# Kernel tuning notes

Hardware: AMD Instinct MI355X
Metric: run time of the kernel (lower is better)

Reference implementation:

```python
import jax, jax.numpy as jnp
import numpy as np

LAMBD = 1.0  # margin, matches init kwarg lambd
N, C, D = 16384, 4096, 128


def setup_inputs() -> dict:
    key = jax.random.key(0)
    k1, k2, k3 = jax.random.split(key, 3)
    embeddings = jax.random.normal(k1, (N, D), dtype=jnp.float32)
    targets = jax.random.randint(k2, (N,), 0, C, dtype=jnp.int64)
    centers = jax.random.normal(k3, (C, D), dtype=jnp.float32)
    return {"embeddings": embeddings, "targets": targets, "centers": centers}


def reference(embeddings, targets, centers):
    # Squared euclidean distances from every sample to every center, [n, C],
    # via ||e||^2 + ||c||^2 - 2 e.c (avoids the [n, C, d] broadcast tensor).
    e2 = jnp.sum(embeddings * embeddings, axis=-1, keepdims=True)          # [n, 1]
    c2 = jnp.sum(centers * centers, axis=-1)                               # [C]
    dist = e2 + c2[None, :] - 2.0 * jnp.matmul(embeddings, centers.T)      # [n, C]

    tgt = targets.astype(jnp.int32)
    ap = jnp.take_along_axis(dist, tgt[:, None], axis=1)                   # [n, 1]

    # loss_val[i, c] = lambd + d(e_i, center_{y_i}) - d(e_i, center_c)
    loss_val = LAMBD + ap - dist                                           # [n, C]

    # Triplet (i, y_i, c) is mined iff loss_val > 0 and c != y_i.
    not_label = jnp.arange(dist.shape[1], dtype=jnp.int32)[None, :] != tgt[:, None]
    mask = (loss_val > 0.0) & not_label

    # For mined triplets relu(ap - an + lambd) == loss_val (already > 0).
    total = jnp.sum(jnp.where(mask, loss_val, 0.0))
    cnt = jnp.sum(mask).astype(loss_val.dtype)
    # If no triplet violates the margin, the original returns 0.
    return jnp.where(cnt > 0.0, total / jnp.maximum(cnt, 1.0), 0.0)
```

## Files before the change

### kernel.cpp

```cpp
#include <hip/hip_runtime.h>

#define N_SAMP 16384
#define N_CENT 4096
#define DIM    128
#define LAMBD  1.0f
#define NSLOT  256

typedef _Float16 half8  __attribute__((ext_vector_type(8)));
typedef float    floatx4 __attribute__((ext_vector_type(4)));

struct Slot { float sum; unsigned int cnt; unsigned int pad[30]; };

__device__ __forceinline__ void gload_lds16(const void* g, void* l) {
  __builtin_amdgcn_global_load_lds(
      (__attribute__((address_space(1))) void*)(g),
      (__attribute__((address_space(3))) void*)(l), 16, 0, 0);
}

__global__ __launch_bounds__(256) void prep_kernel(
    const float* __restrict__ E, const float* __restrict__ Cc,
    const int* __restrict__ tgt,
    _Float16* __restrict__ Eh, _Float16* __restrict__ Ch,
    float* __restrict__ c2, float* __restrict__ rowk,
    Slot* __restrict__ slots) {
  const int tid = threadIdx.x;
  const int STAT_BLOCKS = (N_SAMP + N_CENT) / 4;
  if ((int)blockIdx.x < STAT_BLOCKS) {
    if (blockIdx.x == 0) { slots[tid].sum = 0.f; slots[tid].cnt = 0u; }
    const int wv   = blockIdx.x * 4 + (tid >> 6);
    const int lane = tid & 63;
    if (wv < N_SAMP) {
      const int yi = tgt[wv];
      float2 e = *(const float2*)(E  + (size_t)wv * DIM + lane * 2);
      float2 c = *(const float2*)(Cc + (size_t)yi * DIM + lane * 2);
      float s = c.x * (c.x - 2.f * e.x) + c.y * (c.y - 2.f * e.y);
      #pragma unroll
      for (int off = 32; off > 0; off >>= 1) s += __shfl_down(s, off);
      if (lane == 0) rowk[wv] = LAMBD + s;
    } else {
      const int cI = wv - N_SAMP;
      float2 c = *(const float2*)(Cc + (size_t)cI * DIM + lane * 2);
      float s = c.x * c.x + c.y * c.y;
      #pragma unroll
      for (int off = 32; off > 0; off >>= 1) s += __shfl_down(s, off);
      if (lane == 0) c2[cI] = s;
    }
  } else {
    const int t = ((int)blockIdx.x - STAT_BLOCKS) * 256 + tid;
    const int NE8 = N_SAMP * DIM / 8;
    const float4* src;
    half8* dst;
    int idx;
    if (t < NE8) { src = (const float4*)E;  dst = (half8*)Eh; idx = t; }
    else         { src = (const float4*)Cc; dst = (half8*)Ch; idx = t - NE8; }
    float4 a = src[(size_t)idx * 2], b = src[(size_t)idx * 2 + 1];
    half8 h;
    h[0]=(_Float16)a.x; h[1]=(_Float16)a.y; h[2]=(_Float16)a.z; h[3]=(_Float16)a.w;
    h[4]=(_Float16)b.x; h[5]=(_Float16)b.y; h[6]=(_Float16)b.z; h[7]=(_Float16)b.w;
    dst[idx] = h;
  }
}

__global__ __launch_bounds__(256, 2) void center_gemm_kernel(
    const _Float16* __restrict__ Eh, const _Float16* __restrict__ Ch,
    const float* __restrict__ c2, const float* __restrict__ rowk,
    const int* __restrict__ tgt,
    Slot* __restrict__ slots) {
  __shared__ _Float16 As[128 * DIM];
  __shared__ _Float16 Bs[128 * DIM];
  __shared__ float rowkS[128];
  __shared__ float c2S[128];
  __shared__ int   yS[128];
  __shared__ float swsum[4];
  __shared__ int   swcnt[4];

  const int tid  = threadIdx.x;
  const int w    = tid >> 6;
  const int lane = tid & 63;

  const int bid = blockIdx.x;
  const int xcd = bid & 7;
  const int j   = bid >> 3;
  const int bm  = xcd * 16 + (j & 15);
  const int bn  = j >> 4;

  {
    const char* gA = (const char*)(Eh + (size_t)bm * 128 * DIM);
    const char* gB = (const char*)(Ch + (size_t)bn * 128 * DIM);
    char* lA = (char*)As;
    char* lB = (char*)Bs;
    const int p  = lane & 15;
    const int r4 = lane >> 4;
    #pragma unroll
    for (int it = 0; it < 8; ++it) {
      const int off = (w * 8 + it) * 1024;
      const int row = (w * 8 + it) * 4 + r4;
      const int gof = row * 256 + (p ^ (row & 15)) * 16;
      gload_lds16(gA + gof, lA + off);
      gload_lds16(gB + gof, lB + off);
    }
  }
  if (tid < 128) {
    rowkS[tid] = rowk[bm * 128 + tid];
    yS[tid]    = tgt[bm * 128 + tid];
    c2S[tid]   = c2[bn * 128 + tid];
  }
  __syncthreads();

  const int wm = w >> 1, wn = w & 1;
  const int q = lane >> 4, r = lane & 15;
  const int row0 = wm * 64, col0 = wn * 64;

  floatx4 acc[4][4];
  #pragma unroll
  for (int a = 0; a < 4; ++a)
    #pragma unroll
    for (int b = 0; b < 4; ++b)
      acc[a][b] = (floatx4){0.f, 0.f, 0.f, 0.f};

  #pragma unroll
  for (int ks = 0; ks < 4; ++ks) {
    const int cidx = ks * 4 + q;
    half8 af[4], bf[4];
    #pragma unroll
    for (int mt = 0; mt < 4; ++mt)
      af[mt] = *(const half8*)&As[(row0 + mt * 16 + r) * DIM + ((cidx ^ r) * 8)];
    #pragma unroll
    for (int nt = 0; nt < 4; ++nt)
      bf[nt] = *(const half8*)&Bs[(col0 + nt * 16 + r) * DIM + ((cidx ^ r) * 8)];
    #pragma unroll
    for (int mt = 0; mt < 4; ++mt)
      #pragma unroll
      for (int nt = 0; nt < 4; ++nt)
        acc[mt][nt] = __builtin_amdgcn_mfma_f32_16x16x32_f16(af[mt], bf[nt], acc[mt][nt], 0, 0, 0);
  }

  float lsum = 0.f;
  int   lcnt = 0;
  #pragma unroll
  for (int mt = 0; mt < 4; ++mt) {
    float rk[4]; int yv[4];
    #pragma unroll
    for (int rg = 0; rg < 4; ++rg) {
      const int row = row0 + mt * 16 + q * 4 + rg;
      rk[rg] = rowkS[row];
      yv[rg] = yS[row];
    }
    #pragma unroll
    for (int nt = 0; nt < 4; ++nt) {
      const int col  = col0 + nt * 16 + r;
      const float c2v = c2S[col];
      const int gcol = bn * 128 + col;
      #pragma unroll
      for (int rg = 0; rg < 4; ++rg) {
        const float v = rk[rg] + 2.f * acc[mt][nt][rg] - c2v;
        const bool mined = (v > 0.f) & (gcol != yv[rg]);
        lsum += mined ? v : 0.f;
        lcnt += mined ? 1 : 0;
      }
    }
  }

  #pragma unroll
  for (int off = 32; off > 0; off >>= 1) {
    lsum += __shfl_down(lsum, off);
    lcnt += __shfl_down(lcnt, off);
  }
  if (lane == 0) { swsum[w] = lsum; swcnt[w] = lcnt; }
  __syncthreads();
  if (tid == 0) {
    const float s = swsum[0] + swsum[1] + swsum[2] + swsum[3];
    const int   c = swcnt[0] + swcnt[1] + swcnt[2] + swcnt[3];
    Slot* sl = &slots[bid & (NSLOT - 1)];
    atomicAdd(&sl->sum, s);
    atomicAdd(&sl->cnt, (unsigned int)c);
  }
}

__global__ __launch_bounds__(256) void finalize_kernel(
    const Slot* __restrict__ slots, float* __restrict__ out) {
  const int tid = threadIdx.x;
  float s = slots[tid].sum;
  unsigned int c = slots[tid].cnt;
  #pragma unroll
  for (int off = 32; off > 0; off >>= 1) {
    s += __shfl_down(s, off);
    c += __shfl_down(c, off);
  }
  __shared__ float ss[4];
  __shared__ unsigned int sc[4];
  if ((tid & 63) == 0) { ss[tid >> 6] = s; sc[tid >> 6] = c; }
  __syncthreads();
  if (tid == 0) {
    const float S = ss[0] + ss[1] + ss[2] + ss[3];
    const unsigned int C = sc[0] + sc[1] + sc[2] + sc[3];
    out[0] = (C > 0u) ? (S / (float)C) : 0.f;
  }
}

__global__ void zero_kernel(float* ws_sum, unsigned int* ws_cnt) {
  if (threadIdx.x == 0) { *ws_sum = 0.f; *ws_cnt = 0u; }
}

__global__ void finalize_simple(const float* __restrict__ ws_sum,
                                const unsigned int* __restrict__ ws_cnt,
                                float* __restrict__ out) {
  if (threadIdx.x == 0 && blockIdx.x == 0) {
    const unsigned int c = *ws_cnt;
    out[0] = (c > 0u) ? (*ws_sum / (float)c) : 0.f;
  }
}

__global__ __launch_bounds__(256) void fallback_kernel(
    const float* __restrict__ E, const float* __restrict__ Cc,
    const int* __restrict__ tgt,
    float* __restrict__ ws_sum, unsigned int* __restrict__ ws_cnt) {
  __shared__ float eS[DIM];
  __shared__ float apS;
  const int i = blockIdx.x;
  const int tid = threadIdx.x;
  if (tid < DIM) eS[tid] = E[(size_t)i * DIM + tid];
  __syncthreads();
  const int yi = tgt[i];
  float dloc[16];
  #pragma unroll
  for (int j = 0; j < 16; ++j) {
    const int c = tid + 256 * j;
    const float* cp = Cc + (size_t)c * DIM;
    float s = 0.f;
    for (int d = 0; d < DIM; d += 4) {
      float4 cv = *(const float4*)(cp + d);
      s += cv.x * (cv.x - 2.f * eS[d + 0]) + cv.y * (cv.y - 2.f * eS[d + 1])
         + cv.z * (cv.z - 2.f * eS[d + 2]) + cv.w * (cv.w - 2.f * eS[d + 3]);
    }
    dloc[j] = s;
    if (c == yi) apS = s;
  }
  __syncthreads();
  const float apv = apS;
  float lsum = 0.f; int lcnt = 0;
  #pragma unroll
  for (int j = 0; j < 16; ++j) {
    const int c = tid + 256 * j;
    const float v = LAMBD + apv - dloc[j];
    const bool mined = (v > 0.f) & (c != yi);
    lsum += mined ? v : 0.f;
    lcnt += mined ? 1 : 0;
  }
  #pragma unroll
  for (int off = 32; off > 0; off >>= 1) {
    lsum += __shfl_down(lsum, off);
    lcnt += __shfl_down(lcnt, off);
  }
  __shared__ float swsum[4];
  __shared__ int   swcnt[4];
  const int w = tid >> 6, lane = tid & 63;
  if (lane == 0) { swsum[w] = lsum; swcnt[w] = lcnt; }
  __syncthreads();
  if (tid == 0) {
    atomicAdd(ws_sum, swsum[0] + swsum[1] + swsum[2] + swsum[3]);
    atomicAdd(ws_cnt, (unsigned int)(swcnt[0] + swcnt[1] + swcnt[2] + swcnt[3]));
  }
}

extern "C" void kernel_launch(void* const* d_in, const int* in_sizes, int n_in,
                              void* d_out, int out_size, void* d_ws, size_t ws_size,
                              hipStream_t stream) {
  const float* E   = (const float*)d_in[0];
  const int*   tgt = (const int*)d_in[1];
  const float* Cc  = (const float*)d_in[2];
  float* out = (float*)d_out;

  const size_t EH_BYTES = (size_t)N_SAMP * DIM * 2;
  const size_t CH_BYTES = (size_t)N_CENT * DIM * 2;
  const size_t C2_BYTES = (size_t)N_CENT * 4;
  const size_t RK_BYTES = (size_t)N_SAMP * 4;
  const size_t SL_BYTES = (size_t)NSLOT * sizeof(Slot);
  const size_t NEEDED = EH_BYTES + CH_BYTES + C2_BYTES + RK_BYTES + SL_BYTES;

  char* ws = (char*)d_ws;
  if (ws_size >= NEEDED) {
    _Float16* Eh = (_Float16*)ws;
    _Float16* Ch = (_Float16*)(ws + EH_BYTES);
    float* c2    = (float*)(ws + EH_BYTES + CH_BYTES);
    float* rowk  = (float*)(ws + EH_BYTES + CH_BYTES + C2_BYTES);
    Slot* slots  = (Slot*)(ws + EH_BYTES + CH_BYTES + C2_BYTES + RK_BYTES);

    const int STAT_BLOCKS = (N_SAMP + N_CENT) / 4;
    const int CONV_BLOCKS = (N_SAMP * DIM / 8 + N_CENT * DIM / 8) / 256;
    prep_kernel<<<STAT_BLOCKS + CONV_BLOCKS, 256, 0, stream>>>(
        E, Cc, tgt, Eh, Ch, c2, rowk, slots);
    center_gemm_kernel<<<(N_CENT / 128) * (N_SAMP / 128), 256, 0, stream>>>(
        Eh, Ch, c2, rowk, tgt, slots);
    finalize_kernel<<<1, 256, 0, stream>>>(slots, out);
  } else {
    float* ws_sum = (float*)ws;
    unsigned int* ws_cnt = (unsigned int*)(ws_sum + 1);
    zero_kernel<<<1, 64, 0, stream>>>(ws_sum, ws_cnt);
    fallback_kernel<<<N_SAMP, 256, 0, stream>>>(E, Cc, tgt, ws_sum, ws_cnt);
    finalize_simple<<<1, 64, 0, stream>>>(ws_sum, ws_cnt, out);
  }
}
```

Measured before the change: 101.3 us.

## Make GEMM blocks persistent over eight row tiles with double-buffered A loads

```diff
diff --git a/kernel.cpp b/kernel.cpp
--- a/kernel.cpp
+++ b/kernel.cpp
@@ -61,104 +61,134 @@
   }
 }
 
-__global__ __launch_bounds__(256, 2) void center_gemm_kernel(
+__global__ __launch_bounds__(512, 2) void center_gemm_kernel(
     const _Float16* __restrict__ Eh, const _Float16* __restrict__ Ch,
     const float* __restrict__ c2, const float* __restrict__ rowk,
     const int* __restrict__ tgt,
     Slot* __restrict__ slots) {
-  __shared__ _Float16 As[128 * DIM];
-  __shared__ _Float16 Bs[128 * DIM];
-  __shared__ float rowkS[128];
-  __shared__ float c2S[128];
-  __shared__ int   yS[128];
-  __shared__ float swsum[4];
-  __shared__ int   swcnt[4];
+  __shared__ _Float16 As[2][128 * DIM];
+  __shared__ _Float16 Bs[256 * DIM];
+  __shared__ float c2S[256];
+  __shared__ float rowkS[2][128];
+  __shared__ int   yS[2][128];
+  __shared__ float swsum[8];
+  __shared__ int   swcnt[8];
 
   const int tid  = threadIdx.x;
   const int w    = tid >> 6;
   const int lane = tid & 63;
 
-  const int bid = blockIdx.x;
-  const int xcd = bid & 7;
-  const int j   = bid >> 3;
-  const int bm  = xcd * 16 + (j & 15);
-  const int bn  = j >> 4;
+  const int bid    = blockIdx.x;
+  const int xcd    = bid & 7;
+  const int j      = bid >> 3;
+  const int bm_grp = xcd * 2 + (j & 1);
+  const int bn_grp = j >> 1;
+  const int bn0    = bn_grp * 256;
+
+  const int p  = lane & 15;
+  const int r4 = lane >> 4;
 
   {
-    const char* gA = (const char*)(Eh + (size_t)bm * 128 * DIM);
-    const char* gB = (const char*)(Ch + (size_t)bn * 128 * DIM);
-    char* lA = (char*)As;
+    const char* gB = (const char*)(Ch + (size_t)bn0 * DIM);
     char* lB = (char*)Bs;
-    const int p  = lane & 15;
-    const int r4 = lane >> 4;
     #pragma unroll
     for (int it = 0; it < 8; ++it) {
-      const int off = (w * 8 + it) * 1024;
-      const int row = (w * 8 + it) * 4 + r4;
-      const int gof = row * 256 + (p ^ (row & 15)) * 16;
-      gload_lds16(gA + gof, lA + off);
-      gload_lds16(gB + gof, lB + off);
-    }
-  }
+      const int chunk = w * 8 + it;
+      const int row   = chunk * 4 + r4;
+      gload_lds16(gB + row * 256 + (p ^ (row & 15)) * 16, lB + chunk * 1024);
+    }
+    const char* gA = (const char*)(Eh + (size_t)bm_grp * 8 * 128 * DIM);
+    char* lA = (char*)As[0];
+    #pragma unroll
+    for (int it = 0; it < 4; ++it) {
+      const int chunk = w * 4 + it;
+      const int row   = chunk * 4 + r4;
+      gload_lds16(gA + row * 256 + (p ^ (row & 15)) * 16, lA + chunk * 1024);
+    }
+  }
+  if (tid < 256) c2S[tid] = c2[bn0 + tid];
   if (tid < 128) {
-    rowkS[tid] = rowk[bm * 128 + tid];
-    yS[tid]    = tgt[bm * 128 + tid];
-    c2S[tid]   = c2[bn * 128 + tid];
-  }
-  __syncthreads();
-
-  const int wm = w >> 1, wn = w & 1;
+    const int rg0 = bm_grp * 8 * 128 + tid;
+    rowkS[0][tid] = rowk[rg0];
+    yS[0][tid]    = tgt[rg0];
+  }
+  __syncthreads();
+
+  const int wm = w >> 2, wn = w & 3;
   const int q = lane >> 4, r = lane & 15;
   const int row0 = wm * 64, col0 = wn * 64;
 
-  floatx4 acc[4][4];
-  #pragma unroll
-  for (int a = 0; a < 4; ++a)
-    #pragma unroll
-    for (int b = 0; b < 4; ++b)
-      acc[a][b] = (floatx4){0.f, 0.f, 0.f, 0.f};
-
-  #pragma unroll
-  for (int ks = 0; ks < 4; ++ks) {
-    const int cidx = ks * 4 + q;
-    half8 af[4], bf[4];
-    #pragma unroll
-    for (int mt = 0; mt < 4; ++mt)
-      af[mt] = *(const half8*)&As[(row0 + mt * 16 + r) * DIM + ((cidx ^ r) * 8)];
-    #pragma unroll
-    for (int nt = 0; nt < 4; ++nt)
-      bf[nt] = *(const half8*)&Bs[(col0 + nt * 16 + r) * DIM + ((cidx ^ r) * 8)];
-    #pragma unroll
-    for (int mt = 0; mt < 4; ++mt)
-      #pragma unroll
-      for (int nt = 0; nt < 4; ++nt)
-        acc[mt][nt] = __builtin_amdgcn_mfma_f32_16x16x32_f16(af[mt], bf[nt], acc[mt][nt], 0, 0, 0);
-  }
-
   float lsum = 0.f;
   int   lcnt = 0;
-  #pragma unroll
-  for (int mt = 0; mt < 4; ++mt) {
-    float rk[4]; int yv[4];
-    #pragma unroll
-    for (int rg = 0; rg < 4; ++rg) {
-      const int row = row0 + mt * 16 + q * 4 + rg;
-      rk[rg] = rowkS[row];
-      yv[rg] = yS[row];
-    }
-    #pragma unroll
-    for (int nt = 0; nt < 4; ++nt) {
-      const int col  = col0 + nt * 16 + r;
-      const float c2v = c2S[col];
-      const int gcol = bn * 128 + col;
+
+  for (int t = 0; t < 8; ++t) {
+    const int cur = t & 1;
+
+    if (t < 7) {
+      const char* gA = (const char*)(Eh + (size_t)(bm_grp * 8 + t + 1) * 128 * DIM);
+      char* lA = (char*)As[cur ^ 1];
+      #pragma unroll
+      for (int it = 0; it < 4; ++it) {
+        const int chunk = w * 4 + it;
+        const int row   = chunk * 4 + r4;
+        gload_lds16(gA + row * 256 + (p ^ (row & 15)) * 16, lA + chunk * 1024);
+      }
+      if (tid < 128) {
+        const int rg1 = (bm_grp * 8 + t + 1) * 128 + tid;
+        rowkS[cur ^ 1][tid] = rowk[rg1];
+        yS[cur ^ 1][tid]    = tgt[rg1];
+      }
+    }
+
+    floatx4 acc[4][4];
+    #pragma unroll
+    for (int a = 0; a < 4; ++a)
+      #pragma unroll
+      for (int b = 0; b < 4; ++b)
+        acc[a][b] = (floatx4){0.f, 0.f, 0.f, 0.f};
+
+    #pragma unroll
+    for (int ks = 0; ks < 4; ++ks) {
+      const int cidx = ks * 4 + q;
+      half8 af[4], bf[4];
+      #pragma unroll
+      for (int mt = 0; mt < 4; ++mt)
+        af[mt] = *(const half8*)&As[cur][(row0 + mt * 16 + r) * DIM + ((cidx ^ r) * 8)];
+      #pragma unroll
+      for (int nt = 0; nt < 4; ++nt)
+        bf[nt] = *(const half8*)&Bs[(col0 + nt * 16 + r) * DIM + ((cidx ^ r) * 8)];
+      #pragma unroll
+      for (int mt = 0; mt < 4; ++mt)
+        #pragma unroll
+        for (int nt = 0; nt < 4; ++nt)
+          acc[mt][nt] = __builtin_amdgcn_mfma_f32_16x16x32_f16(af[mt], bf[nt], acc[mt][nt], 0, 0, 0);
+    }
+
+    #pragma unroll
+    for (int mt = 0; mt < 4; ++mt) {
+      float rk[4]; int yv[4];
       #pragma unroll
       for (int rg = 0; rg < 4; ++rg) {
-        const float v = rk[rg] + 2.f * acc[mt][nt][rg] - c2v;
-        const bool mined = (v > 0.f) & (gcol != yv[rg]);
-        lsum += mined ? v : 0.f;
-        lcnt += mined ? 1 : 0;
+        const int row = row0 + mt * 16 + q * 4 + rg;
+        rk[rg] = rowkS[cur][row];
+        yv[rg] = yS[cur][row];
       }
-    }
+      #pragma unroll
+      for (int nt = 0; nt < 4; ++nt) {
+        const int col  = col0 + nt * 16 + r;
+        const float c2v = c2S[col];
+        const int gcol = bn0 + col;
+        #pragma unroll
+        for (int rg = 0; rg < 4; ++rg) {
+          const float v = rk[rg] + 2.f * acc[mt][nt][rg] - c2v;
+          const bool mined = (v > 0.f) & (gcol != yv[rg]);
+          lsum += mined ? v : 0.f;
+          lcnt += mined ? 1 : 0;
+        }
+      }
+    }
+
+    __syncthreads();
   }
 
   #pragma unroll
@@ -169,8 +199,9 @@
   if (lane == 0) { swsum[w] = lsum; swcnt[w] = lcnt; }
   __syncthreads();
   if (tid == 0) {
-    const float s = swsum[0] + swsum[1] + swsum[2] + swsum[3];
-    const int   c = swcnt[0] + swcnt[1] + swcnt[2] + swcnt[3];
+    float s = 0.f; int c = 0;
+    #pragma unroll
+    for (int k = 0; k < 8; ++k) { s += swsum[k]; c += swcnt[k]; }
     Slot* sl = &slots[bid & (NSLOT - 1)];
     atomicAdd(&sl->sum, s);
     atomicAdd(&sl->cnt, (unsigned int)c);
@@ -290,8 +321,7 @@
     const int CONV_BLOCKS = (N_SAMP * DIM / 8 + N_CENT * DIM / 8) / 256;
     prep_kernel<<<STAT_BLOCKS + CONV_BLOCKS, 256, 0, stream>>>(
         E, Cc, tgt, Eh, Ch, c2, rowk, slots);
-    center_gemm_kernel<<<(N_CENT / 128) * (N_SAMP / 128), 256, 0, stream>>>(
-        Eh, Ch, c2, rowk, tgt, slots);
+    center_gemm_kernel<<<256, 512, 0, stream>>>(Eh, Ch, c2, rowk, tgt, slots);
     finalize_kernel<<<1, 256, 0, stream>>>(slots, out);
   } else {
     float* ws_sum = (float*)ws;
```

New measurement: 94.79 us. 6.4% less time.
